# Optimization experiments

Measured on AMD Instinct MI355X. Metric: run time of the kernel, lower is better.

The kernel has to match this reference:

```python
import jax, jax.numpy as jnp
import numpy as np

B, S, D, H, DFF = 2, 2048, 1024, 16, 4096
DK = D // H
EPS = float(np.finfo(np.float32).eps)  # torch RMSNorm default eps = finfo eps


def rmsnorm(x, g):
    var = jnp.mean(x * x, axis=-1, keepdims=True)
    return x * jax.lax.rsqrt(var + EPS) * g


def rope_cos_sin(seq_len, dim, base=10000.0):
    inv_freq = 1.0 / (base ** (jnp.arange(0, dim, 2, dtype=jnp.float32) / dim))
    t = jnp.arange(seq_len, dtype=jnp.float32)
    freqs = jnp.outer(t, inv_freq)            # [S, dim/2]
    emb = jnp.concatenate([freqs, freqs], -1)  # [S, dim]
    return jnp.cos(emb), jnp.sin(emb)


def rotate_half(x):
    x1, x2 = x[..., : x.shape[-1] // 2], x[..., x.shape[-1] // 2:]
    return jnp.concatenate([-x2, x1], axis=-1)


def setup_inputs() -> dict:
    key = jax.random.key(0)
    ks = jax.random.split(key, 16)
    sc = 0.02
    return {
        "x": jax.random.normal(ks[0], (B, S, D), jnp.float32),
        "wq": jax.random.normal(ks[1], (D, D), jnp.float32) * sc,
        "bq": jnp.zeros((D,), jnp.float32),
        "wk": jax.random.normal(ks[2], (D, D), jnp.float32) * sc,
        "bk": jnp.zeros((D,), jnp.float32),
        "wv": jax.random.normal(ks[3], (D, D), jnp.float32) * sc,
        "bv": jnp.zeros((D,), jnp.float32),
        "wo": jax.random.normal(ks[4], (D, D), jnp.float32) * sc,
        "bo": jnp.zeros((D,), jnp.float32),
        "w1": jax.random.normal(ks[5], (D, DFF), jnp.float32) * sc,
        "b1": jnp.zeros((DFF,), jnp.float32),
        "w2": jax.random.normal(ks[6], (DFF, D), jnp.float32) * sc,
        "b2": jnp.zeros((D,), jnp.float32),
        "g1": jnp.ones((D,), jnp.float32),
        "g2": jnp.ones((D,), jnp.float32),
    }


def reference(x, wq, bq, wk, bk, wv, bv, wo, bo, w1, b1, w2, b2, g1, g2):
    b, s, d = x.shape
    # --- self-attention sublayer (pre-RMSNorm residual) ---
    h = rmsnorm(x, g1)
    q = (h @ wq + bq).reshape(b, s, H, DK).transpose(0, 2, 1, 3)  # [B,H,S,dk]
    k = (h @ wk + bk).reshape(b, s, H, DK).transpose(0, 2, 1, 3)
    v = (h @ wv + bv).reshape(b, s, H, DK).transpose(0, 2, 1, 3)
    cos, sin = rope_cos_sin(s, DK)
    cos = cos[None, None]  # [1,1,S,dk]
    sin = sin[None, None]
    q = q * cos + rotate_half(q) * sin
    k = k * cos + rotate_half(k) * sin
    scores = jnp.einsum("bhqd,bhkd->bhqk", q, k) / jnp.sqrt(jnp.float32(DK))
    p = jax.nn.softmax(scores, axis=-1)
    o = jnp.einsum("bhqk,bhkd->bhqd", p, v)
    o = o.transpose(0, 2, 1, 3).reshape(b, s, d)
    attn_out = o @ wo + bo
    x = x + attn_out
    # --- feed-forward sublayer ---
    h2 = rmsnorm(x, g2)
    ff = jax.nn.relu(h2 @ w1 + b1) @ w2 + b2
    return x + ff
```

## Files before the change

### kernel.cpp

```cpp
#include <hip/hip_runtime.h>
#include <math.h>

typedef unsigned short u16;
typedef __attribute__((ext_vector_type(8))) short bf16x8;
typedef __attribute__((ext_vector_type(4))) float f32x4;
typedef __attribute__((ext_vector_type(4))) unsigned int u32x4;

#define B_ 2
#define S_ 2048
#define D_ 1024
#define H_ 16
#define DK_ 64
#define DFF_ 4096
#define EPS_ 1.1920928955078125e-07f
#define EXP2SC 0.18033688011112042f

__device__ __forceinline__ float bf2f(u16 u) {
  unsigned int v = ((unsigned int)u) << 16;
  return __builtin_bit_cast(float, v);
}
__device__ __forceinline__ u16 f2bf(float f) {
  unsigned int x = __builtin_bit_cast(unsigned int, f);
  x += 0x7fffu + ((x >> 16) & 1u);
  return (u16)(x >> 16);
}

typedef __attribute__((address_space(3))) unsigned int lds_uint;
typedef const __attribute__((address_space(1))) unsigned int glb_uint;
__device__ __forceinline__ void gload16(const void* g, void* l) {
  __builtin_amdgcn_global_load_lds((glb_uint*)g, (lds_uint*)l, 16, 0, 0);
}

__device__ __forceinline__ unsigned int cvtpk(float lo, float hi) {
  unsigned int d;
  asm("v_cvt_pk_bf16_f32 %0, %1, %2" : "=v"(d) : "v"(lo), "v"(hi));
  return d;
}
__device__ __forceinline__ void plswap32(unsigned int& a, unsigned int& b) {
  asm("v_permlane32_swap_b32 %0, %1" : "+v"(a), "+v"(b));
}
__device__ __forceinline__ void plswap16(unsigned int& a, unsigned int& b) {
  asm("v_permlane16_swap_b32 %0, %1" : "+v"(a), "+v"(b));
}

__device__ __forceinline__ void xcd_swizzle(int& bx, int& by) {
  const int nx = gridDim.x;
  const int nwg = nx * gridDim.y;
  const int lin = blockIdx.y * nx + blockIdx.x;
  const int swz = (lin & 7) * (nwg >> 3) + (lin >> 3);
  bx = swz % nx;
  by = swz / nx;
}

__global__ __launch_bounds__(256) void prep_qkvo(
    const float* __restrict__ wq, const float* __restrict__ wk,
    const float* __restrict__ wv, const float* __restrict__ wo,
    u16* __restrict__ qkvT, u16* __restrict__ woT,
    float* __restrict__ cosT, float* __restrict__ sinT) {
  __shared__ float t[32][33];
  const int bid = blockIdx.x;
  const int tid = threadIdx.x;
  if (bid < 4096) {
    const int m = bid >> 10;
    const int tb = bid & 1023;
    const float* src = (m == 0) ? wq : (m == 1) ? wk : (m == 2) ? wv : wo;
    u16* dst = (m == 3) ? woT : qkvT + (size_t)m * D_ * D_;
    const int c0 = (tb & 31) * 32, r0 = (tb >> 5) * 32;
    const int tx = tid & 31, ty = tid >> 5;
#pragma unroll
    for (int i = 0; i < 32; i += 8)
      t[ty + i][tx] = src[(size_t)(r0 + ty + i) * D_ + (c0 + tx)];
    __syncthreads();
#pragma unroll
    for (int i = 0; i < 32; i += 8)
      dst[(size_t)(c0 + ty + i) * D_ + (r0 + tx)] = f2bf(t[tx][ty + i]);
  } else {
    const int idx = (bid - 4096) * 256 + tid;
    const int s = idx >> 5, i = idx & 31;
    double inv = exp(((double)(-2 * i) / (double)DK_) * log(10000.0));
    double ang = (double)s * inv;
    cosT[idx] = (float)cos(ang);
    sinT[idx] = (float)sin(ang);
  }
}

__global__ __launch_bounds__(256) void prep_w12(
    const float* __restrict__ w1, const float* __restrict__ w2,
    u16* __restrict__ w1T, u16* __restrict__ w2T) {
  __shared__ float t[32][33];
  const int bid = blockIdx.x;
  const int tid = threadIdx.x;
  const int tx = tid & 31, ty = tid >> 5;
  if (bid < 4096) {
    const int c0 = (bid & 127) * 32, r0 = (bid >> 7) * 32;
#pragma unroll
    for (int i = 0; i < 32; i += 8)
      t[ty + i][tx] = w1[(size_t)(r0 + ty + i) * DFF_ + (c0 + tx)];
    __syncthreads();
#pragma unroll
    for (int i = 0; i < 32; i += 8)
      w1T[(size_t)(c0 + ty + i) * D_ + (r0 + tx)] = f2bf(t[tx][ty + i]);
  } else {
    const int b2 = bid - 4096;
    const int c0 = (b2 & 31) * 32, r0 = (b2 >> 5) * 32;
#pragma unroll
    for (int i = 0; i < 32; i += 8)
      t[ty + i][tx] = w2[(size_t)(r0 + ty + i) * D_ + (c0 + tx)];
    __syncthreads();
#pragma unroll
    for (int i = 0; i < 32; i += 8)
      w2T[(size_t)(c0 + ty + i) * DFF_ + (r0 + tx)] = f2bf(t[tx][ty + i]);
  }
}

__global__ __launch_bounds__(256) void rmsnorm_k(const float* __restrict__ X,
                                                 const float* __restrict__ g,
                                                 u16* __restrict__ out) {
  const int row = blockIdx.x;
  const float* xr = X + (size_t)row * D_;
  u16* orow = out + (size_t)row * D_;
  const int tid = threadIdx.x;
  float vals[4];
  float s = 0.f;
#pragma unroll
  for (int j = 0; j < 4; j++) {
    float v = xr[tid + j * 256];
    vals[j] = v;
    s += v * v;
  }
#pragma unroll
  for (int off = 32; off > 0; off >>= 1) s += __shfl_down(s, off, 64);
  __shared__ float red[4];
  __shared__ float ssc;
  int lane = tid & 63, wave = tid >> 6;
  if (lane == 0) red[wave] = s;
  __syncthreads();
  if (tid == 0) ssc = 1.0f / sqrtf((red[0] + red[1] + red[2] + red[3]) * (1.0f / D_) + EPS_);
  __syncthreads();
  float sc = ssc;
#pragma unroll
  for (int j = 0; j < 4; j++) {
    int i = tid + j * 256;
    orow[i] = f2bf(vals[j] * sc * g[i]);
  }
}

#define GK_STAGE(BU, K0)                                                               \
  _Pragma("unroll")                                                                    \
  for (int c = wave; c < BM / 16; c += 4) {                                            \
    const u16* gp = gkA + (size_t)(m0 + c * 16 + lrow) * gkLD + (K0) + lcol;           \
    gload16(gp, (char*)As + __builtin_amdgcn_readfirstlane((BU) * (BM * 64) + c * 1024)); \
  }                                                                                    \
  _Pragma("unroll")                                                                    \
  for (int c = wave; c < BN / 16; c += 4) {                                            \
    const u16* gp = gkB + (size_t)(n0 + c * 16 + lrow) * gkLD + (K0) + lcol;           \
    gload16(gp, (char*)Bs + __builtin_amdgcn_readfirstlane((BU) * (BN * 64) + c * 1024)); \
  }

#define GK_COMPUTE(BU)                                                                 \
  {                                                                                    \
    bf16x8 af[WR], bfv[WC];                                                            \
    _Pragma("unroll")                                                                  \
    for (int i = 0; i < WR; i++)                                                       \
      af[i] = *(const bf16x8*)&As[(BU) * (BM * 32) + (wm + i * 16 + l16) * 32 + quad * 8]; \
    _Pragma("unroll")                                                                  \
    for (int j = 0; j < WC; j++)                                                       \
      bfv[j] = *(const bf16x8*)&Bs[(BU) * (BN * 32) + (wn + j * 16 + l16) * 32 + quad * 8]; \
    _Pragma("unroll")                                                                  \
    for (int i = 0; i < WR; i++)                                                       \
      _Pragma("unroll")                                                                \
      for (int j = 0; j < WC; j++)                                                     \
        acc[i][j] = __builtin_amdgcn_mfma_f32_16x16x32_bf16(af[i], bfv[j], acc[i][j], 0, 0, 0); \
  }

#define GEMM_KLOOP(APTR, BPTR, KLEN, KLD)                                              \
  {                                                                                    \
    const u16* gkA = (APTR);                                                           \
    const u16* gkB = (BPTR);                                                           \
    const int gkLD = (KLD);                                                            \
    GK_STAGE(0, 0)                                                                     \
    for (int k0 = 0; k0 < (KLEN); k0 += 64) {                                          \
      __syncthreads();               \
      GK_STAGE(1, k0 + 32)                       \
      GK_COMPUTE(0)                                                                    \
      __syncthreads();                    \
      if (k0 + 64 < (KLEN)) { GK_STAGE(0, k0 + 64) }                                   \
      GK_COMPUTE(1)                                                                    \
    }                                                                                  \
  }

template <int MODE, int WR, int WC>
__global__ __launch_bounds__(256) void gemm_bt(
    const u16* __restrict__ A, const u16* __restrict__ Bt, const float* __restrict__ bias,
    u16* __restrict__ outB, float* __restrict__ outF, const float* __restrict__ resF,
    int M, int N, int K) {
  constexpr int BM = 2 * WR * 16;
  constexpr int BN = 2 * WC * 16;
  __shared__ u16 As[BM * 64];
  __shared__ u16 Bs[BN * 64];
  const int tid = threadIdx.x;
  const int wave = tid >> 6, lane = tid & 63, quad = lane >> 4, l16 = lane & 15;
  const int wm = (wave >> 1) * (WR * 16), wn = (wave & 1) * (WC * 16);
  int bx, by;
  xcd_swizzle(bx, by);
  const int m0 = by * BM, n0 = bx * BN;
  const int lrow = lane >> 2, lcol = (lane & 3) * 8;
  f32x4 acc[WR][WC] = {};
  GEMM_KLOOP(A, Bt, K, K)
#pragma unroll
  for (int i = 0; i < WR; i++)
#pragma unroll
    for (int j = 0; j < WC; j++) {
      int col = n0 + wn + j * 16 + l16;
      float bv = bias[col];
#pragma unroll
      for (int r = 0; r < 4; r++) {
        int row = m0 + wm + i * 16 + quad * 4 + r;
        size_t off = (size_t)row * N + col;
        float v = acc[i][j][r] + bv;
        if constexpr (MODE == 1) v = fmaxf(v, 0.f);
        if constexpr (MODE == 2) outF[off] = v + resF[off];
        else outB[off] = f2bf(v);
      }
    }
}

__global__ __launch_bounds__(256) void gemm_qkv(
    const u16* __restrict__ A, const u16* __restrict__ Bt,
    const float* __restrict__ bq, const float* __restrict__ bk, const float* __restrict__ bv,
    const float* __restrict__ cosT, const float* __restrict__ sinT,
    u16* __restrict__ Qb, u16* __restrict__ Kb, u16* __restrict__ VT, int M, int K) {
  constexpr int WR = 4, WC = 4;
  constexpr int BM = 128, BN = 128;
  __shared__ u16 As[BM * 64];
  __shared__ u16 Bs[BN * 64];
  const int tid = threadIdx.x;
  const int wave = tid >> 6, lane = tid & 63, quad = lane >> 4, l16 = lane & 15;
  const int wm = (wave >> 1) * 64, wn = (wave & 1) * 64;
  int bx, by;
  xcd_swizzle(bx, by);
  const int m0 = by * BM, n0 = bx * BN;
  const int lrow = lane >> 2, lcol = (lane & 3) * 8;
  f32x4 acc[WR][WC] = {};
  GEMM_KLOOP(A, Bt, K, K)
  const int g = n0 >> 10;
  if (g < 2) {
    u16* dst = (g == 0) ? Qb : Kb;
    const float* bias = (g == 0) ? bq : bk;
    const float scq = (g == 0) ? EXP2SC : 1.0f;
#pragma unroll
    for (int i = 0; i < WR; i++)
#pragma unroll
      for (int jp = 0; jp < 2; jp++) {
        int col0 = n0 + wn + jp * 16 + l16;
        int c0 = col0 & 1023;
        float bv0 = bias[c0], bv1 = bias[c0 + 32];
        int irot = jp * 16 + l16;
        int row0 = m0 + wm + i * 16 + quad * 4;
#pragma unroll
        for (int r = 0; r < 4; r++) {
          int row = row0 + r;
          int s2 = row & 2047;
          float cs = cosT[s2 * 32 + irot];
          float sn = sinT[s2 * 32 + irot];
          float x0 = acc[i][jp][r] + bv0;
          float x1 = acc[i][jp + 2][r] + bv1;
          dst[(size_t)row * D_ + c0]      = f2bf((x0 * cs - x1 * sn) * scq);
          dst[(size_t)row * D_ + c0 + 32] = f2bf((x1 * cs + x0 * sn) * scq);
        }
      }
  } else {
#pragma unroll
    for (int i = 0; i < WR; i++)
#pragma unroll
      for (int j = 0; j < WC; j++) {
        int col = n0 + wn + j * 16 + l16;
        int c = col & 1023;
        float bvv = bv[c];
        int row0 = m0 + wm + i * 16 + quad * 4;
        int hh = c >> 6, dk = c & 63;
        int b = row0 >> 11, s2 = row0 & 2047;
        ushort4 pv;
        pv.x = f2bf(acc[i][j][0] + bvv);
        pv.y = f2bf(acc[i][j][1] + bvv);
        pv.z = f2bf(acc[i][j][2] + bvv);
        pv.w = f2bf(acc[i][j][3] + bvv);
        *(ushort4*)&VT[(((size_t)(b * H_ + hh)) * DK_ + dk) * S_ + s2] = pv;
      }
  }
}

template <int WR, int WC>
__global__ __launch_bounds__(256) void gemm_splitk(
    const u16* __restrict__ A, const u16* __restrict__ Bt, const float* __restrict__ bias,
    float* outF, int M, int N, int Kslice, int Kld) {
  constexpr int BM = 2 * WR * 16;
  constexpr int BN = 2 * WC * 16;
  __shared__ u16 As[BM * 64];
  __shared__ u16 Bs[BN * 64];
  const int tid = threadIdx.x;
  const int wave = tid >> 6, lane = tid & 63, quad = lane >> 4, l16 = lane & 15;
  const int wm = (wave >> 1) * (WR * 16), wn = (wave & 1) * (WC * 16);
  int bx, by;
  xcd_swizzle(bx, by);
  const int m0 = by * BM, n0 = bx * BN;
  const int lrow = lane >> 2, lcol = (lane & 3) * 8;
  const u16* Ao = A + (size_t)blockIdx.z * Kslice;
  const u16* Bo = Bt + (size_t)blockIdx.z * Kslice;
  f32x4 acc[WR][WC] = {};
  GEMM_KLOOP(Ao, Bo, Kslice, Kld)
  const bool addb = (blockIdx.z == 0);
#pragma unroll
  for (int i = 0; i < WR; i++)
#pragma unroll
    for (int j = 0; j < WC; j++) {
      int col = n0 + wn + j * 16 + l16;
      float bv = addb ? bias[col] : 0.f;
#pragma unroll
      for (int r = 0; r < 4; r++) {
        int row = m0 + wm + i * 16 + quad * 4 + r;
        unsafeAtomicAdd(&outF[(size_t)row * N + col], acc[i][j][r] + bv);
      }
    }
}

__device__ __forceinline__ void softmax_pack(f32x4 s0, f32x4 s1, f32x4 s2, f32x4 s3,
                                             bf16x8& pf0, bf16x8& pf1) {
  f32x4 p0, p1, p2, p3;
#pragma unroll
  for (int r = 0; r < 4; r++) {
    p0[r] = exp2f(s0[r]);
    p1[r] = exp2f(s1[r]);
    p2[r] = exp2f(s2[r]);
    p3[r] = exp2f(s3[r]);
  }
  unsigned int X0 = cvtpk(p0[0], p0[1]), X1 = cvtpk(p0[2], p0[3]);
  unsigned int Y0 = cvtpk(p1[0], p1[1]), Y1 = cvtpk(p1[2], p1[3]);
  unsigned int Z0 = cvtpk(p2[0], p2[1]), Z1 = cvtpk(p2[2], p2[3]);
  unsigned int W0 = cvtpk(p3[0], p3[1]), W1 = cvtpk(p3[2], p3[3]);
  plswap32(X0, Y0); plswap16(X0, Y0);
  plswap32(X1, Y1); plswap16(X1, Y1);
  plswap32(Z0, W0); plswap16(Z0, W0);
  plswap32(Z1, W1); plswap16(Z1, W1);
  u32x4 lo = {X0, X1, Y0, Y1};
  u32x4 hi = {Z0, Z1, W0, W1};
  pf0 = __builtin_bit_cast(bf16x8, lo);
  pf1 = __builtin_bit_cast(bf16x8, hi);
}

__global__ __launch_bounds__(256, 2) void flash_attn(u16* __restrict__ Q,
                                                     const u16* __restrict__ Kg,
                                                     const u16* __restrict__ VT) {
  const int bh = blockIdx.y;
  const int b = bh >> 4, h = bh & 15;
  const int q0 = blockIdx.x * 128;
  const int tid = threadIdx.x;
  const int wave = tid >> 6, lane = tid & 63, quad = lane >> 4, l16 = lane & 15;
  const size_t base = (size_t)b * S_ * D_ + h * DK_;
  const size_t vbase = (size_t)bh * DK_ * S_;

  __shared__ u16 Ks[2][8192];
  __shared__ u16 Vts[2][8192];

  const int kkey = wave * 32 + (lane >> 3);
  const int kcol = ((lane & 7) ^ (lane >> 3)) * 8;
  const u16* kp0 = Kg + base + (size_t)kkey * D_ + kcol;
  const int vdk0 = wave * 16 + (lane >> 4);
  const int vsel = lane & 15;
  const u16* vp0 = VT + vbase + (size_t)vdk0 * S_;

#define STAGE(BU, KT)                                                                  \
  _Pragma("unroll")                                                                    \
  for (int c = 0; c < 4; c++) {                                                        \
    gload16(kp0 + (size_t)((KT) + c * 8) * D_,                                         \
            (char*)Ks + __builtin_amdgcn_readfirstlane((BU) * 16384 + wave * 4096 + c * 1024)); \
    int vdk = vdk0 + c * 4;                                                            \
    gload16(vp0 + (size_t)(c * 4) * S_ + (KT) + ((vsel ^ (vdk & 7)) * 8),              \
            (char*)Vts + __builtin_amdgcn_readfirstlane((BU) * 16384 + wave * 4096 + c * 1024)); \
  }

  STAGE(0, 0)

  const size_t qoffA = base + (size_t)(q0 + wave * 32 + l16) * D_ + quad * 8;
  const size_t qoffB = qoffA + (size_t)16 * D_;
  bf16x8 qa0 = *(const bf16x8*)(Q + qoffA);
  bf16x8 qa1 = *(const bf16x8*)(Q + qoffA + 32);
  bf16x8 qb0 = *(const bf16x8*)(Q + qoffB);
  bf16x8 qb1 = *(const bf16x8*)(Q + qoffB + 32);

  f32x4 oa[4] = {}, ob[4] = {};
  f32x4 lsa_acc = {}, lsb_acc = {};
  const u32x4 onesu = {0x3F803F80u, 0x3F803F80u, 0x3F803F80u, 0x3F803F80u};
  const bf16x8 ones = __builtin_bit_cast(bf16x8, onesu);
  const int sw = (l16 & 7) << 4;

#define TILE(BU)                                                                       \
  {                                                                                    \
    const char* KsB = (const char*)Ks + (BU) * 16384;                                  \
    const char* VtsB = (const char*)Vts + (BU) * 16384;                                \
    f32x4 sa[2][4] = {}, sb[2][4] = {};                                                \
    __builtin_amdgcn_s_setprio(1);                                                     \
    _Pragma("unroll")                                                                  \
    for (int half = 0; half < 2; half++) {                                             \
      _Pragma("unroll")                                                                \
      for (int nt = 0; nt < 4; nt++) {                                                 \
        const int kr = half * 64 + nt * 16 + l16;                                      \
        const char* krow = KsB + kr * 128;                                             \
        bf16x8 k0 = *(const bf16x8*)(krow + ((quad * 16) ^ sw));                       \
        bf16x8 k1 = *(const bf16x8*)(krow + ((64 + quad * 16) ^ sw));                  \
        sa[half][nt] = __builtin_amdgcn_mfma_f32_16x16x32_bf16(k0, qa0, sa[half][nt], 0, 0, 0); \
        sa[half][nt] = __builtin_amdgcn_mfma_f32_16x16x32_bf16(k1, qa1, sa[half][nt], 0, 0, 0); \
        sb[half][nt] = __builtin_amdgcn_mfma_f32_16x16x32_bf16(k0, qb0, sb[half][nt], 0, 0, 0); \
        sb[half][nt] = __builtin_amdgcn_mfma_f32_16x16x32_bf16(k1, qb1, sb[half][nt], 0, 0, 0); \
      }                                                                                \
    }                                                                                  \
    __builtin_amdgcn_s_setprio(0);                                                     \
    bf16x8 pa[2][2], pb[2][2];                                                         \
    _Pragma("unroll")                                                                  \
    for (int half = 0; half < 2; half++) {                                             \
      softmax_pack(sa[half][0], sa[half][1], sa[half][2], sa[half][3], pa[half][0], pa[half][1]); \
      softmax_pack(sb[half][0], sb[half][1], sb[half][2], sb[half][3], pb[half][0], pb[half][1]); \
    }                                                                                  \
    __builtin_amdgcn_s_setprio(1);                                                     \
    _Pragma("unroll")                                                                  \
    for (int half = 0; half < 2; half++) {                                             \
      lsa_acc = __builtin_amdgcn_mfma_f32_16x16x32_bf16(pa[half][0], ones, lsa_acc, 0, 0, 0); \
      lsa_acc = __builtin_amdgcn_mfma_f32_16x16x32_bf16(pa[half][1], ones, lsa_acc, 0, 0, 0); \
      lsb_acc = __builtin_amdgcn_mfma_f32_16x16x32_bf16(pb[half][0], ones, lsb_acc, 0, 0, 0); \
      lsb_acc = __builtin_amdgcn_mfma_f32_16x16x32_bf16(pb[half][1], ones, lsb_acc, 0, 0, 0); \
      _Pragma("unroll")                                                                \
      for (int nt = 0; nt < 4; nt++) {                                                 \
        const int vr = nt * 16 + l16;                                                  \
        const char* vrow = VtsB + vr * 256;                                            \
        bf16x8 v0 = *(const bf16x8*)(vrow + ((half * 128 + quad * 16) ^ sw));          \
        bf16x8 v1 = *(const bf16x8*)(vrow + ((half * 128 + 64 + quad * 16) ^ sw));     \
        oa[nt] = __builtin_amdgcn_mfma_f32_16x16x32_bf16(pa[half][0], v0, oa[nt], 0, 0, 0); \
        oa[nt] = __builtin_amdgcn_mfma_f32_16x16x32_bf16(pa[half][1], v1, oa[nt], 0, 0, 0); \
        ob[nt] = __builtin_amdgcn_mfma_f32_16x16x32_bf16(pb[half][0], v0, ob[nt], 0, 0, 0); \
        ob[nt] = __builtin_amdgcn_mfma_f32_16x16x32_bf16(pb[half][1], v1, ob[nt], 0, 0, 0); \
      }                                                                                \
    }                                                                                  \
    __builtin_amdgcn_s_setprio(0);                                                     \
  }

  for (int kt = 0; kt < S_; kt += 256) {
    __syncthreads();
    STAGE(1, kt + 128)
    TILE(0)
    __syncthreads();
    if (kt + 256 < S_) { STAGE(0, kt + 256) }
    TILE(1)
  }
#undef STAGE
#undef TILE

#pragma unroll
  for (int r = 0; r < 4; r++) {
    float inva = 1.0f / lsa_acc[r];
    float invb = 1.0f / lsb_acc[r];
    const size_t aoff = base + (size_t)(q0 + wave * 32 + quad * 4 + r) * D_;
    const size_t boff = aoff + (size_t)16 * D_;
#pragma unroll
    for (int nt = 0; nt < 4; nt++) {
      Q[aoff + nt * 16 + l16] = f2bf(oa[nt][r] * inva);
      Q[boff + nt * 16 + l16] = f2bf(ob[nt][r] * invb);
    }
  }
}

extern "C" void kernel_launch(void* const* d_in, const int* in_sizes, int n_in,
                              void* d_out, int out_size, void* d_ws, size_t ws_size,
                              hipStream_t stream) {
  const float* x  = (const float*)d_in[0];
  const float* wq = (const float*)d_in[1];
  const float* bq = (const float*)d_in[2];
  const float* wk = (const float*)d_in[3];
  const float* bk = (const float*)d_in[4];
  const float* wv = (const float*)d_in[5];
  const float* bv = (const float*)d_in[6];
  const float* wo = (const float*)d_in[7];
  const float* bo = (const float*)d_in[8];
  const float* w1 = (const float*)d_in[9];
  const float* b1 = (const float*)d_in[10];
  const float* w2 = (const float*)d_in[11];
  const float* b2 = (const float*)d_in[12];
  const float* g1 = (const float*)d_in[13];
  const float* g2 = (const float*)d_in[14];

  char* ws = (char*)d_ws;
  const size_t MB = 1024 * 1024;
  u16* qkvT = (u16*)(ws + 0 * MB);
  u16* woT  = (u16*)(ws + 6 * MB);
  u16* h    = (u16*)(ws + 8 * MB);
  u16* Qb   = (u16*)(ws + 16 * MB);
  u16* Kb   = (u16*)(ws + 24 * MB);
  float* cosT = (float*)(ws + 32 * MB);
  float* sinT = (float*)(ws + 32 * MB + 256 * 1024);
  u16* w2T  = (u16*)(ws + 0 * MB);
  u16* w1T  = (u16*)(ws + 16 * MB);
  u16* f1   = (u16*)(ws + 24 * MB);
  u16* h2   = h;
  u16* Ob   = Qb;
  u16* VT   = (u16*)d_out;
  float* x2 = (float*)d_out;
  const bool bigffn = (ws_size >= 57 * MB);

  const int MS = B_ * S_;
  prep_qkvo<<<4096 + S_ * 32 / 256, 256, 0, stream>>>(wq, wk, wv, wo, qkvT, woT, cosT, sinT);
  rmsnorm_k<<<MS, 256, 0, stream>>>(x, g1, h);
  gemm_qkv<<<dim3(3 * D_ / 128, MS / 128), 256, 0, stream>>>(h, qkvT, bq, bk, bv, cosT, sinT, Qb, Kb, VT, MS, D_);
  flash_attn<<<dim3(S_ / 128, B_ * H_), 256, 0, stream>>>(Qb, Kb, VT);
  gemm_bt<2, 4, 2><<<dim3(D_ / 64, MS / 128), 256, 0, stream>>>(Ob, woT, bo, nullptr, x2, x, MS, D_, D_);

  prep_w12<<<8192, 256, 0, stream>>>(w1, w2, w1T, w2T);
  rmsnorm_k<<<MS, 256, 0, stream>>>(x2, g2, h2);
  if (bigffn) {
    gemm_bt<1, 4, 4><<<dim3(DFF_ / 128, MS / 128), 256, 0, stream>>>(h2, w1T, b1, f1, nullptr, nullptr, MS, DFF_, D_);
    gemm_splitk<4, 4><<<dim3(D_ / 128, MS / 128, 2), 256, 0, stream>>>(f1, w2T, b2, x2, MS, D_, 2048, DFF_);
  } else {
    for (int i = 0; i < 2; i++) {
      const u16* h2h = h2 + (size_t)i * 2048 * D_;
      float* x2h = x2 + (size_t)i * 2048 * D_;
      gemm_bt<1, 4, 4><<<dim3(DFF_ / 128, 2048 / 128), 256, 0, stream>>>(h2h, w1T, b1, f1, nullptr, nullptr, 2048, DFF_, D_);
      gemm_splitk<4, 4><<<dim3(D_ / 128, 2048 / 128, 4), 256, 0, stream>>>(f1, w2T, b2, x2h, 2048, D_, 1024, DFF_);
    }
  }
  (void)in_sizes; (void)n_in; (void)out_size;
}
```

Baseline: 385.8 us.

## Double-buffer GEMM K-loop with 64-wide stages and explicit vmcnt waits

Reworks the shared GEMM K-loop from two 32-wide half-buffers, where each stage was issued just before the compute that needed it, into two full 64-wide buffers. Loads now run one whole iteration ahead, and partial s_waitcnt vmcnt waits replace __syncthreads so the next stage's global-to-LDS loads stay in flight during compute. This is meant to hide global memory latency behind the MFMA work. In exchange it doubles LDS per block, which can lower occupancy, and it depends on hand-counted vmcnt values matching the number of loads issued per stage.

```diff
diff --git a/kernel.cpp b/kernel.cpp
--- a/kernel.cpp
+++ b/kernel.cpp
@@ -29,6 +29,13 @@
 typedef const __attribute__((address_space(1))) unsigned int glb_uint;
 __device__ __forceinline__ void gload16(const void* g, void* l) {
   __builtin_amdgcn_global_load_lds((glb_uint*)g, (lds_uint*)l, 16, 0, 0);
+}
+
+template <int N>
+__device__ __forceinline__ void waitcnt_vm() {
+  if constexpr (N == 8) asm volatile("s_waitcnt vmcnt(8)" ::: "memory");
+  else if constexpr (N == 6) asm volatile("s_waitcnt vmcnt(6)" ::: "memory");
+  else asm volatile("s_waitcnt vmcnt(0)" ::: "memory");
 }
 
 __device__ __forceinline__ unsigned int cvtpk(float lo, float hi) {
@@ -147,25 +154,29 @@
 
 #define GK_STAGE(BU, K0)                                                               \
   _Pragma("unroll")                                                                    \
-  for (int c = wave; c < BM / 16; c += 4) {                                            \
-    const u16* gp = gkA + (size_t)(m0 + c * 16 + lrow) * gkLD + (K0) + lcol;           \
-    gload16(gp, (char*)As + __builtin_amdgcn_readfirstlane((BU) * (BM * 64) + c * 1024)); \
-  }                                                                                    \
+  for (int p = 0; p < 2; p++) {                                                        \
+    _Pragma("unroll")                                                                  \
+    for (int c = wave; c < BM / 16; c += 4) {                                          \
+      const u16* gp = gkA + (size_t)(m0 + c * 16 + lrow) * gkLD + (K0) + p * 32 + lcol; \
+      gload16(gp, (char*)As + __builtin_amdgcn_readfirstlane((BU) * (BM * 128) + p * (BM * 64) + c * 1024)); \
+    }                                                                                  \
+    _Pragma("unroll")                                                                  \
+    for (int c = wave; c < BN / 16; c += 4) {                                          \
+      const u16* gp = gkB + (size_t)(n0 + c * 16 + lrow) * gkLD + (K0) + p * 32 + lcol; \
+      gload16(gp, (char*)Bs + __builtin_amdgcn_readfirstlane((BU) * (BN * 128) + p * (BN * 64) + c * 1024)); \
+    }                                                                                  \
+  }
+
+#define GK_COMPUTE(BU)                                                                 \
   _Pragma("unroll")                                                                    \
-  for (int c = wave; c < BN / 16; c += 4) {                                            \
-    const u16* gp = gkB + (size_t)(n0 + c * 16 + lrow) * gkLD + (K0) + lcol;           \
-    gload16(gp, (char*)Bs + __builtin_amdgcn_readfirstlane((BU) * (BN * 64) + c * 1024)); \
-  }
-
-#define GK_COMPUTE(BU)                                                                 \
-  {                                                                                    \
+  for (int p = 0; p < 2; p++) {                                                        \
     bf16x8 af[WR], bfv[WC];                                                            \
     _Pragma("unroll")                                                                  \
     for (int i = 0; i < WR; i++)                                                       \
-      af[i] = *(const bf16x8*)&As[(BU) * (BM * 32) + (wm + i * 16 + l16) * 32 + quad * 8]; \
+      af[i] = *(const bf16x8*)&As[(BU) * (BM * 64) + p * (BM * 32) + (wm + i * 16 + l16) * 32 + quad * 8]; \
     _Pragma("unroll")                                                                  \
     for (int j = 0; j < WC; j++)                                                       \
-      bfv[j] = *(const bf16x8*)&Bs[(BU) * (BN * 32) + (wn + j * 16 + l16) * 32 + quad * 8]; \
+      bfv[j] = *(const bf16x8*)&Bs[(BU) * (BN * 64) + p * (BN * 32) + (wn + j * 16 + l16) * 32 + quad * 8]; \
     _Pragma("unroll")                                                                  \
     for (int i = 0; i < WR; i++)                                                       \
       _Pragma("unroll")                                                                \
@@ -179,13 +190,16 @@
     const u16* gkB = (BPTR);                                                           \
     const int gkLD = (KLD);                                                            \
     GK_STAGE(0, 0)                                                                     \
+    GK_STAGE(1, 64)                                                                    \
+    int gkcur = 0;                                                                     \
     for (int k0 = 0; k0 < (KLEN); k0 += 64) {                                          \
-      __syncthreads();               \
-      GK_STAGE(1, k0 + 32)                       \
-      GK_COMPUTE(0)                                                                    \
-      __syncthreads();                    \
-      if (k0 + 64 < (KLEN)) { GK_STAGE(0, k0 + 64) }                                   \
-      GK_COMPUTE(1)                                                                    \
+      if (k0 + 64 < (KLEN)) waitcnt_vm<WR + WC>();   \
+      else waitcnt_vm<0>();                                      \
+      __builtin_amdgcn_s_barrier();                                                    \
+      GK_COMPUTE(gkcur)                                                                \
+      __builtin_amdgcn_s_barrier();                         \
+      if (k0 + 128 < (KLEN)) { GK_STAGE(gkcur, k0 + 128) }                             \
+      gkcur ^= 1;                                                                      \
     }                                                                                  \
   }
 
@@ -196,8 +210,8 @@
     int M, int N, int K) {
   constexpr int BM = 2 * WR * 16;
   constexpr int BN = 2 * WC * 16;
-  __shared__ u16 As[BM * 64];
-  __shared__ u16 Bs[BN * 64];
+  __shared__ u16 As[2 * BM * 64];
+  __shared__ u16 Bs[2 * BN * 64];
   const int tid = threadIdx.x;
   const int wave = tid >> 6, lane = tid & 63, quad = lane >> 4, l16 = lane & 15;
   const int wm = (wave >> 1) * (WR * 16), wn = (wave & 1) * (WC * 16);
@@ -232,8 +246,8 @@
     u16* __restrict__ Qb, u16* __restrict__ Kb, u16* __restrict__ VT, int M, int K) {
   constexpr int WR = 4, WC = 4;
   constexpr int BM = 128, BN = 128;
-  __shared__ u16 As[BM * 64];
-  __shared__ u16 Bs[BN * 64];
+  __shared__ u16 As[2 * BM * 64];
+  __shared__ u16 Bs[2 * BN * 64];
   const int tid = threadIdx.x;
   const int wave = tid >> 6, lane = tid & 63, quad = lane >> 4, l16 = lane & 15;
   const int wm = (wave >> 1) * 64, wn = (wave & 1) * 64;
@@ -296,8 +310,8 @@
     float* outF, int M, int N, int Kslice, int Kld) {
   constexpr int BM = 2 * WR * 16;
   constexpr int BN = 2 * WC * 16;
-  __shared__ u16 As[BM * 64];
-  __shared__ u16 Bs[BN * 64];
+  __shared__ u16 As[2 * BM * 64];
+  __shared__ u16 Bs[2 * BN * 64];
   const int tid = threadIdx.x;
   const int wave = tid >> 6, lane = tid & 63, quad = lane >> 4, l16 = lane & 15;
   const int wm = (wave >> 1) * (WR * 16), wn = (wave & 1) * (WC * 16);
```

New measurement: 363.3 us. 5.8% less time.
